# Kernel optimization log

Hardware: AMD Instinct MI355X
Metric: run time of the kernel (lower is better)

## Reference

```python
import jax, jax.numpy as jnp
import numpy as np

NUM_HEADS = 8
NUM_POINTS = 4
NUM_PIP = 4  # num_points_in_pillar
RADIUS = 0.12


def grid_sample_bilinear(feat, grid):
    """torch.nn.functional.grid_sample(mode='bilinear', padding_mode='zeros', align_corners=False).
    feat: [G, D, H, W], grid: [G, Q, P, 2] in [-1, 1] (x=width, y=height) -> [G, Q, P, D]."""
    G, D, H, W = feat.shape
    Q, P = grid.shape[1], grid.shape[2]
    x = (grid[..., 0] + 1.0) * 0.5 * W - 0.5
    y = (grid[..., 1] + 1.0) * 0.5 * H - 0.5
    x0 = jnp.floor(x)
    y0 = jnp.floor(y)
    feat_flat = feat.reshape(G, D, H * W).transpose(0, 2, 1)  # [G, HW, D]
    out = jnp.zeros((G, Q * P, D), dtype=feat.dtype)
    for dx, dy in ((0, 0), (1, 0), (0, 1), (1, 1)):
        xi = x0 + dx
        yi = y0 + dy
        w = (1.0 - jnp.abs(x - xi)) * (1.0 - jnp.abs(y - yi))
        valid = (xi >= 0) & (xi <= W - 1) & (yi >= 0) & (yi <= H - 1)
        xi_c = jnp.clip(xi, 0, W - 1).astype(jnp.int32)
        yi_c = jnp.clip(yi, 0, H - 1).astype(jnp.int32)
        idx = (yi_c * W + xi_c).reshape(G, Q * P)
        g = jnp.take_along_axis(feat_flat, idx[:, :, None], axis=1)  # [G, Q*P, D]
        out = out + g * (w * valid.astype(w.dtype)).reshape(G, Q * P, 1)
    return out.reshape(G, Q, P, D)


def setup_inputs() -> dict:
    key = jax.random.key(0)
    ks = jax.random.split(key, 8)
    B, N, C = 1, 2500, 256
    cams, H, W = 6, 46, 80
    return {
        "query": jax.random.normal(ks[0], (B, N, C), dtype=jnp.float32),
        "image_feats": jax.random.normal(ks[1], (B, cams, C, H, W), dtype=jnp.float32),
        "reference_points_cam": jax.random.uniform(ks[2], (B, cams, N, NUM_PIP, 2), dtype=jnp.float32),
        "bev_mask": jax.random.uniform(ks[3], (B, cams, N, NUM_PIP)) > 0.3,
        "offset_w": jax.random.normal(ks[4], (NUM_HEADS * NUM_PIP * NUM_POINTS * 2, C), dtype=jnp.float32) * 0.02,
        "offset_b": jnp.zeros((NUM_HEADS * NUM_PIP * NUM_POINTS * 2,), dtype=jnp.float32),
        "weight_w": jax.random.normal(ks[5], (NUM_HEADS * NUM_PIP * NUM_POINTS, C), dtype=jnp.float32) * 0.02,
        "weight_b": jnp.zeros((NUM_HEADS * NUM_PIP * NUM_POINTS,), dtype=jnp.float32),
        "out_w": jax.random.normal(ks[6], (C, C), dtype=jnp.float32) * 0.02,
        "out_b": jnp.zeros((C,), dtype=jnp.float32),
    }


def reference(query, image_feats, reference_points_cam, bev_mask,
              offset_w, offset_b, weight_w, weight_b, out_w, out_b):
    B, N, C = query.shape
    cams, H, W = image_feats.shape[1], image_feats.shape[3], image_feats.shape[4]
    heads, PiP, P = NUM_HEADS, NUM_PIP, NUM_POINTS
    K = PiP * P
    D = C // heads

    # Per-query learned offsets and attention logits
    offsets = jnp.tanh(query @ offset_w.T + offset_b).reshape(B, N, heads, PiP, P, 2) * RADIUS
    wl = (query @ weight_w.T + weight_b).reshape(B, N, heads, K)  # [B,N,h,K]

    # Sampling locations per camera: ref [B,cams,N,PiP,2] + offsets -> [B,cams,N,h,K,2]
    loc = reference_points_cam[:, :, :, None, :, None, :] + offsets[:, None]
    loc = loc.reshape(B, cams, N, heads, K, 2)

    # Visibility mask broadcast to points: [B,cams,N,h,K]
    vis = jnp.broadcast_to(bev_mask[:, :, :, None, :, None], (B, cams, N, heads, PiP, P))
    vis = vis.reshape(B, cams, N, heads, K)

    # Masked softmax over K (handles fully-masked rows)
    m = vis.astype(wl.dtype)
    logits = jnp.where(vis, wl[:, None], jnp.asarray(-1e9, wl.dtype))
    w = jax.nn.softmax(logits, axis=-1) * m
    w = w / jnp.clip(jnp.sum(w, axis=-1, keepdims=True), 1e-6)

    # grid_sample over all (batch, cam, head) at once
    grid = loc.transpose(0, 1, 3, 2, 4, 5).reshape(B * cams * heads, N, K, 2) * 2.0 - 1.0
    feat = image_feats.reshape(B * cams * heads, D, H, W)
    sampled = grid_sample_bilinear(feat, grid)  # [B*cams*h, N, K, D]
    sampled = sampled.reshape(B, cams, heads, N, K, D).transpose(0, 1, 3, 2, 4, 5)  # [B,cams,N,h,K,D]

    cam_out = jnp.sum(sampled * w[..., None], axis=4).reshape(B, cams, N, C)

    has_vis = jnp.any(bev_mask, axis=-1)  # [B,cams,N]
    cam_out = cam_out * has_vis[..., None].astype(cam_out.dtype)

    fused = jnp.sum(cam_out, axis=1)  # [B,N,C]
    counts = jnp.clip(jnp.sum(has_vis.astype(jnp.int32), axis=1), 1)  # [B,N]
    fused = fused / counts[..., None].astype(fused.dtype)
    return fused @ out_w.T + out_b
```

## Files before the change

kernel.cpp:

```cpp
#include <hip/hip_runtime.h>
#include <math.h>

#define CAMS 6
#define CCH 256
#define HH 46
#define WW 80
#define NPIX (HH * WW)
#define HEADS 8
#define PIP 4
#define PP 4
#define KK 16
#define RADIUS_F 0.12f
#define NC 384

__device__ __forceinline__ unsigned short f2bf(float f) {
    unsigned int x = __float_as_uint(f);
    unsigned int r = (x + 0x7FFFu + ((x >> 16) & 1u)) >> 16;
    return (unsigned short)r;
}
__device__ __forceinline__ float bf2f(unsigned short u) {
    return __uint_as_float(((unsigned int)u) << 16);
}

__global__ void __launch_bounds__(256) feat_transpose_k(const float* __restrict__ in,
                                                        unsigned short* __restrict__ out) {
    __shared__ float tile[64][65];
    int cam = blockIdx.z;
    int r0 = blockIdx.y * 64;
    int p0 = blockIdx.x * 64;
    int tj = threadIdx.x & 63;
    int ti = threadIdx.x >> 6;
    const float* src = in + ((long)cam * CCH + r0) * NPIX + p0;
#pragma unroll
    for (int k = 0; k < 64; k += 4) {
        if (p0 + tj < NPIX) tile[ti + k][tj] = src[(long)(ti + k) * NPIX + tj];
    }
    __syncthreads();
    unsigned short* dst = out + ((long)cam * NPIX + p0) * CCH + r0;
#pragma unroll
    for (int k = 0; k < 64; k += 4) {
        if (p0 + ti + k < NPIX) dst[(long)(ti + k) * CCH + tj] = f2bf(tile[tj][ti + k]);
    }
}

__global__ void __launch_bounds__(256) wtrans_k(const float* __restrict__ offw,
                                                const float* __restrict__ ww,
                                                const float* __restrict__ outw,
                                                float* __restrict__ WC,
                                                float* __restrict__ outT) {
    __shared__ float tile[64][65];
    int b = blockIdx.x;
    const float* src;
    float* dst;
    int C, tr, tc, dstride, dcol0;
    if (b < 16)      { src = offw; dst = WC;   C = 256; tr = b >> 2;        tc = b & 3;        dstride = NC;  dcol0 = 0; }
    else if (b < 24) { src = ww;   dst = WC;   C = 256; tr = (b - 16) >> 2; tc = (b - 16) & 3; dstride = NC;  dcol0 = 256; }
    else             { src = outw; dst = outT; C = 256; tr = (b - 24) >> 2; tc = (b - 24) & 3; dstride = 256; dcol0 = 0; }
    if (b >= 16 && b < 24) { tr = (b - 16) & 1; tc = (b - 16) >> 1; }
    int tj = threadIdx.x & 63;
    int ti = threadIdx.x >> 6;
#pragma unroll
    for (int k = 0; k < 64; k += 4)
        tile[ti + k][tj] = src[(long)(tr * 64 + ti + k) * C + tc * 64 + tj];
    __syncthreads();
#pragma unroll
    for (int k = 0; k < 64; k += 4)
        dst[(long)(tc * 64 + ti + k) * dstride + dcol0 + tr * 64 + tj] = tile[tj][ti + k];
}

__global__ void __launch_bounds__(256) qgemm3_k(const float* __restrict__ query,
                                                const float* __restrict__ WC,
                                                const float* __restrict__ offB,
                                                const float* __restrict__ wB,
                                                float* __restrict__ offsets,
                                                float* __restrict__ wl,
                                                int N) {
    __shared__ float qt[64][32][4];
    int t = threadIdx.x;
    int w = t >> 6, l = t & 63;
    int m0 = blockIdx.x * 32;
    int col = blockIdx.y * 64 + l;

#pragma unroll
    for (int i = 0; i < 8; i++) {
        int mm = i * 4 + w;
        int gm = m0 + mm;
        float4 v = make_float4(0.f, 0.f, 0.f, 0.f);
        if (gm < N) v = *(const float4*)(query + (long)gm * CCH + (l << 2));
        *(float4*)&qt[l][mm ^ (l & 31)][0] = v;
    }
    __syncthreads();

    int mb = w * 8;
    float acc[8] = {0.f, 0.f, 0.f, 0.f, 0.f, 0.f, 0.f, 0.f};
#pragma unroll 2
    for (int jg = 0; jg < 64; jg++) {
        const float* rp = WC + (long)(jg * 4) * NC + col;
        float w0 = rp[0];
        float w1 = rp[NC];
        float w2 = rp[2 * NC];
        float w3 = rp[3 * NC];
        int sw = jg & 31;
#pragma unroll
        for (int r = 0; r < 8; r++) {
            const float4 qv = *(const float4*)&qt[jg][(mb + r) ^ sw][0];
            acc[r] = fmaf(qv.w, w3, fmaf(qv.z, w2, fmaf(qv.y, w1, fmaf(qv.x, w0, acc[r]))));
        }
    }

    if (col < 256) {
        float b = offB[col];
#pragma unroll
        for (int r = 0; r < 8; r++) {
            int gm = m0 + mb + r;
            if (gm < N) offsets[(long)gm * CCH + col] = tanhf(acc[r] + b) * RADIUS_F;
        }
    } else {
        int c2 = col - 256;
        float b = wB[c2];
#pragma unroll
        for (int r = 0; r < 8; r++) {
            int gm = m0 + mb + r;
            if (gm < N) wl[(long)gm * 128 + c2] = acc[r] + b;
        }
    }
}

__global__ void __launch_bounds__(256, 4) sample_cam_k(
        const unsigned short* __restrict__ feat_t,
        const float* __restrict__ refp,
        const int* __restrict__ bev,
        const float* __restrict__ offsets,
        const float* __restrict__ wl,
        float* __restrict__ cam_out,
        int N, int per_xcd) {
    int xcd = blockIdx.x & 7;
    int local = (blockIdx.x >> 3) * 4 + (threadIdx.x >> 6);
    if (local >= per_xcd) return;
    long task = (long)xcd * per_xcd + local;
    if (task >= (long)CAMS * N) return;
    int cam = (int)(task / N);
    int n = (int)(task - (long)cam * N);

    int l = threadIdx.x & 63;
    int h = l >> 3;

    const int* bv = bev + ((long)cam * N + n) * 4;
    int m0 = bv[0], m1 = bv[1], m2 = bv[2], m3 = bv[3];
    float* outp = cam_out + ((long)cam * N + n) * CCH + (l << 2);
    if (!(m0 | m1 | m2 | m3)) {
        *(float4*)outp = make_float4(0.f, 0.f, 0.f, 0.f);
        return;
    }

    const float* rp = refp + ((long)cam * N + n) * 8;
    const float4* offn = (const float4*)(offsets + (long)n * CCH + (h << 5));
    const float4* wln = (const float4*)(wl + (long)n * 128 + (h << 4));

    float4 wl0, wl1, wl2, wl3;
    float mmax = -1e30f;
    if (m0) { wl0 = wln[0]; mmax = fmaxf(mmax, fmaxf(fmaxf(wl0.x, wl0.y), fmaxf(wl0.z, wl0.w))); }
    if (m1) { wl1 = wln[1]; mmax = fmaxf(mmax, fmaxf(fmaxf(wl1.x, wl1.y), fmaxf(wl1.z, wl1.w))); }
    if (m2) { wl2 = wln[2]; mmax = fmaxf(mmax, fmaxf(fmaxf(wl2.x, wl2.y), fmaxf(wl2.z, wl2.w))); }
    if (m3) { wl3 = wln[3]; mmax = fmaxf(mmax, fmaxf(fmaxf(wl3.x, wl3.y), fmaxf(wl3.z, wl3.w))); }

    float w_[KK];
#pragma unroll
    for (int k = 0; k < KK; k++) w_[k] = 0.f;
    float ssum = 0.f;
    if (m0) {
        w_[0] = __expf(wl0.x - mmax); w_[1] = __expf(wl0.y - mmax);
        w_[2] = __expf(wl0.z - mmax); w_[3] = __expf(wl0.w - mmax);
        ssum += w_[0] + w_[1] + w_[2] + w_[3];
    }
    if (m1) {
        w_[4] = __expf(wl1.x - mmax); w_[5] = __expf(wl1.y - mmax);
        w_[6] = __expf(wl1.z - mmax); w_[7] = __expf(wl1.w - mmax);
        ssum += w_[4] + w_[5] + w_[6] + w_[7];
    }
    if (m2) {
        w_[8] = __expf(wl2.x - mmax); w_[9] = __expf(wl2.y - mmax);
        w_[10] = __expf(wl2.z - mmax); w_[11] = __expf(wl2.w - mmax);
        ssum += w_[8] + w_[9] + w_[10] + w_[11];
    }
    if (m3) {
        w_[12] = __expf(wl3.x - mmax); w_[13] = __expf(wl3.y - mmax);
        w_[14] = __expf(wl3.z - mmax); w_[15] = __expf(wl3.w - mmax);
        ssum += w_[12] + w_[13] + w_[14] + w_[15];
    }
    float inv = 1.f / ssum;

    const ushort4* fcam = (const ushort4*)(feat_t + (long)cam * NPIX * CCH) + l;
    float ax = 0.f, ay = 0.f, az = 0.f, aw = 0.f;

#pragma unroll
    for (int pip = 0; pip < PIP; pip++) {
        int vis = (pip == 0) ? m0 : (pip == 1) ? m1 : (pip == 2) ? m2 : m3;
        if (!vis) continue;
        float rx = rp[pip * 2 + 0];
        float ry = rp[pip * 2 + 1];
        float4 oa = offn[pip * 2];
        float4 ob = offn[pip * 2 + 1];
        float px[PP] = {oa.x, oa.z, ob.x, ob.z};
        float py[PP] = {oa.y, oa.w, ob.y, ob.w};
#pragma unroll
        for (int p = 0; p < PP; p++) {
            float wgt = w_[pip * PP + p];
            float x = fmaf(rx + px[p], (float)WW, -0.5f);
            float y = fmaf(ry + py[p], (float)HH, -0.5f);
            float x0f = floorf(x), y0f = floorf(y);
            float fx = x - x0f, fy = y - y0f;
            int ix = (int)x0f, iy = (int)y0f;
            int ix0 = min(max(ix, 0), WW - 1);
            int ix1 = min(max(ix + 1, 0), WW - 1);
            int iy0 = min(max(iy, 0), HH - 1);
            int iy1 = min(max(iy + 1, 0), HH - 1);
            float wx0 = (1.f - fx) * (((ix >= 0) & (ix < WW)) ? 1.f : 0.f);
            float wx1 = fx * (((ix + 1 >= 0) & (ix + 1 < WW)) ? 1.f : 0.f);
            float wy0 = (1.f - fy) * (((iy >= 0) & (iy < HH)) ? 1.f : 0.f);
            float wy1 = fy * (((iy + 1 >= 0) & (iy + 1 < HH)) ? 1.f : 0.f);
            const ushort4 u00 = fcam[(iy0 * WW + ix0) * (CCH / 4)];
            const ushort4 u01 = fcam[(iy0 * WW + ix1) * (CCH / 4)];
            const ushort4 u10 = fcam[(iy1 * WW + ix0) * (CCH / 4)];
            const ushort4 u11 = fcam[(iy1 * WW + ix1) * (CCH / 4)];
            float a00 = wgt * wy0 * wx0;
            float a01 = wgt * wy0 * wx1;
            float a10 = wgt * wy1 * wx0;
            float a11 = wgt * wy1 * wx1;
            ax = fmaf(a00, bf2f(u00.x), ax); ay = fmaf(a00, bf2f(u00.y), ay);
            az = fmaf(a00, bf2f(u00.z), az); aw = fmaf(a00, bf2f(u00.w), aw);
            ax = fmaf(a01, bf2f(u01.x), ax); ay = fmaf(a01, bf2f(u01.y), ay);
            az = fmaf(a01, bf2f(u01.z), az); aw = fmaf(a01, bf2f(u01.w), aw);
            ax = fmaf(a10, bf2f(u10.x), ax); ay = fmaf(a10, bf2f(u10.y), ay);
            az = fmaf(a10, bf2f(u10.z), az); aw = fmaf(a10, bf2f(u10.w), aw);
            ax = fmaf(a11, bf2f(u11.x), ax); ay = fmaf(a11, bf2f(u11.y), ay);
            az = fmaf(a11, bf2f(u11.z), az); aw = fmaf(a11, bf2f(u11.w), aw);
        }
    }
    *(float4*)outp = make_float4(ax * inv, ay * inv, az * inv, aw * inv);
}

__global__ void __launch_bounds__(256) outproj3_k(const float* __restrict__ cam_out,
                                                  const int* __restrict__ bev,
                                                  const float* __restrict__ outT,
                                                  const float* __restrict__ outB,
                                                  float* __restrict__ out, int N) {
    __shared__ float ft[64][32][4];
    __shared__ float inv_s[32];
    int t = threadIdx.x;
    int w = t >> 6, l = t & 63;
    int m0 = blockIdx.x * 32;
    int col = blockIdx.y * 64 + l;

    if (t < 32) {
        int gm = m0 + t;
        int cnt = 0;
        if (gm < N) {
#pragma unroll
            for (int cam = 0; cam < CAMS; cam++) {
                const int* bv = bev + ((long)cam * N + gm) * 4;
                cnt += (bv[0] | bv[1] | bv[2] | bv[3]) ? 1 : 0;
            }
        }
        inv_s[t] = 1.f / (float)max(cnt, 1);
    }

#pragma unroll
    for (int i = 0; i < 8; i++) {
        int mm = i * 4 + w;
        int gm = m0 + mm;
        float4 s = make_float4(0.f, 0.f, 0.f, 0.f);
        if (gm < N) {
#pragma unroll
            for (int cam = 0; cam < CAMS; cam++) {
                const float4 v = *(const float4*)(cam_out + ((long)cam * N + gm) * CCH + (l << 2));
                s.x += v.x; s.y += v.y; s.z += v.z; s.w += v.w;
            }
        }
        *(float4*)&ft[l][mm ^ (l & 31)][0] = s;
    }
    __syncthreads();

    int mb = w * 8;
    float acc[8] = {0.f, 0.f, 0.f, 0.f, 0.f, 0.f, 0.f, 0.f};
#pragma unroll 2
    for (int jg = 0; jg < 64; jg++) {
        const float* rp = outT + (long)(jg * 4) * CCH + col;
        float w0 = rp[0];
        float w1 = rp[CCH];
        float w2 = rp[2 * CCH];
        float w3 = rp[3 * CCH];
        int sw = jg & 31;
#pragma unroll
        for (int r = 0; r < 8; r++) {
            const float4 qv = *(const float4*)&ft[jg][(mb + r) ^ sw][0];
            acc[r] = fmaf(qv.w, w3, fmaf(qv.z, w2, fmaf(qv.y, w1, fmaf(qv.x, w0, acc[r]))));
        }
    }

    float b = outB[col];
#pragma unroll
    for (int r = 0; r < 8; r++) {
        int gm = m0 + mb + r;
        if (gm < N) out[(long)gm * CCH + col] = fmaf(acc[r], inv_s[mb + r], b);
    }
}

extern "C" void kernel_launch(void* const* d_in, const int* in_sizes, int n_in,
                              void* d_out, int out_size, void* d_ws, size_t ws_size,
                              hipStream_t stream) {
    const float* query    = (const float*)d_in[0];
    const float* imfeat   = (const float*)d_in[1];
    const float* refp     = (const float*)d_in[2];
    const int*   bev      = (const int*)d_in[3];
    const float* offset_w = (const float*)d_in[4];
    const float* offset_b = (const float*)d_in[5];
    const float* weight_w = (const float*)d_in[6];
    const float* weight_b = (const float*)d_in[7];
    const float* out_w    = (const float*)d_in[8];
    const float* out_b    = (const float*)d_in[9];
    float* out = (float*)d_out;

    int N = in_sizes[0] / CCH;

    float* ws = (float*)d_ws;
    unsigned short* feat_t = (unsigned short*)ws;
    float* WC     = ws + (size_t)CAMS * NPIX * CCH / 2;
    float* outT   = WC + (size_t)CCH * NC;
    float* offs   = outT + (size_t)CCH * CCH;
    float* wl     = offs + (size_t)N * CCH;
    float* camob  = wl + (size_t)N * 128;

    feat_transpose_k<<<dim3((NPIX + 63) / 64, CCH / 64, CAMS), 256, 0, stream>>>(imfeat, feat_t);
    wtrans_k<<<40, 256, 0, stream>>>(offset_w, weight_w, out_w, WC, outT);

    int mblocks = (N + 31) / 32;
    qgemm3_k<<<dim3(mblocks, 6), 256, 0, stream>>>(query, WC, offset_b, weight_b, offs, wl, N);

    int T = CAMS * N;
    int per_xcd = (T + 7) / 8;
    int blocks = 8 * ((per_xcd + 3) / 4);
    sample_cam_k<<<blocks, 256, 0, stream>>>(feat_t, refp, bev, offs, wl, camob,
                                             N, per_xcd);

    outproj3_k<<<dim3(mblocks, 4), 256, 0, stream>>>(camob, bev, outT, out_b, out, N);
}
```

Before: 97.14 us.

## Merge prep transposes, drop LDS staging in GEMMs, split camera sum

Merges the feature transpose and weight transpose kernels into a single prep launch. The weights are now stored in an interleaved float4 layout so each GEMM lane loads one float4 per k-group. The query and out-projection GEMMs drop their shared-memory staging and read rows straight from global memory with wave-uniform addresses, which should become scalar or broadcast loads. The six-camera sum moves into its own elementwise kernel that writes an intermediate buffer, so there is one extra launch and an extra global round trip in exchange for a simpler out-projection.

```diff
diff --git a/kernel.cpp b/kernel.cpp
--- a/kernel.cpp
+++ b/kernel.cpp
@@ -12,6 +12,7 @@
 #define KK 16
 #define RADIUS_F 0.12f
 #define NC 384
+#define FEATB (58 * 4 * CAMS)
 
 __device__ __forceinline__ unsigned short f2bf(float f) {
     unsigned int x = __float_as_uint(f);
@@ -22,89 +23,79 @@
     return __uint_as_float(((unsigned int)u) << 16);
 }
 
-__global__ void __launch_bounds__(256) feat_transpose_k(const float* __restrict__ in,
-                                                        unsigned short* __restrict__ out) {
+__global__ void __launch_bounds__(256) prep_k(const float* __restrict__ imfeat,
+                                              unsigned short* __restrict__ feat_t,
+                                              const float* __restrict__ offw,
+                                              const float* __restrict__ ww,
+                                              const float* __restrict__ outw,
+                                              float* __restrict__ WCi,
+                                              float* __restrict__ outTi) {
     __shared__ float tile[64][65];
-    int cam = blockIdx.z;
-    int r0 = blockIdx.y * 64;
-    int p0 = blockIdx.x * 64;
+    int b = blockIdx.x;
     int tj = threadIdx.x & 63;
     int ti = threadIdx.x >> 6;
-    const float* src = in + ((long)cam * CCH + r0) * NPIX + p0;
-#pragma unroll
-    for (int k = 0; k < 64; k += 4) {
-        if (p0 + tj < NPIX) tile[ti + k][tj] = src[(long)(ti + k) * NPIX + tj];
-    }
-    __syncthreads();
-    unsigned short* dst = out + ((long)cam * NPIX + p0) * CCH + r0;
-#pragma unroll
-    for (int k = 0; k < 64; k += 4) {
-        if (p0 + ti + k < NPIX) dst[(long)(ti + k) * CCH + tj] = f2bf(tile[tj][ti + k]);
-    }
-}
-
-__global__ void __launch_bounds__(256) wtrans_k(const float* __restrict__ offw,
-                                                const float* __restrict__ ww,
-                                                const float* __restrict__ outw,
-                                                float* __restrict__ WC,
-                                                float* __restrict__ outT) {
-    __shared__ float tile[64][65];
-    int b = blockIdx.x;
-    const float* src;
-    float* dst;
-    int C, tr, tc, dstride, dcol0;
-    if (b < 16)      { src = offw; dst = WC;   C = 256; tr = b >> 2;        tc = b & 3;        dstride = NC;  dcol0 = 0; }
-    else if (b < 24) { src = ww;   dst = WC;   C = 256; tr = (b - 16) >> 2; tc = (b - 16) & 3; dstride = NC;  dcol0 = 256; }
-    else             { src = outw; dst = outT; C = 256; tr = (b - 24) >> 2; tc = (b - 24) & 3; dstride = 256; dcol0 = 0; }
-    if (b >= 16 && b < 24) { tr = (b - 16) & 1; tc = (b - 16) >> 1; }
-    int tj = threadIdx.x & 63;
-    int ti = threadIdx.x >> 6;
-#pragma unroll
-    for (int k = 0; k < 64; k += 4)
-        tile[ti + k][tj] = src[(long)(tr * 64 + ti + k) * C + tc * 64 + tj];
-    __syncthreads();
-#pragma unroll
-    for (int k = 0; k < 64; k += 4)
-        dst[(long)(tc * 64 + ti + k) * dstride + dcol0 + tr * 64 + tj] = tile[tj][ti + k];
-}
-
-__global__ void __launch_bounds__(256) qgemm3_k(const float* __restrict__ query,
-                                                const float* __restrict__ WC,
+    if (b < FEATB) {
+        int px = b % 58, rest = b / 58;
+        int r0 = (rest % 4) * 64;
+        int cam = rest / 4;
+        int p0 = px * 64;
+        const float* src = imfeat + ((long)cam * CCH + r0) * NPIX + p0;
+#pragma unroll
+        for (int k = 0; k < 64; k += 4) {
+            if (p0 + tj < NPIX) tile[ti + k][tj] = src[(long)(ti + k) * NPIX + tj];
+        }
+        __syncthreads();
+        unsigned short* dst = feat_t + ((long)cam * NPIX + p0) * CCH + r0;
+#pragma unroll
+        for (int k = 0; k < 64; k += 4) {
+            if (p0 + ti + k < NPIX) dst[(long)(ti + k) * CCH + tj] = f2bf(tile[tj][ti + k]);
+        }
+    } else {
+        int c = b - FEATB;
+        const float* src;
+        float* dst;
+        int tr, tc, dcols, dcol0;
+        if (c < 16)      { src = offw; dst = WCi;   tr = c >> 2;        tc = c & 3;         dcols = NC;  dcol0 = 0; }
+        else if (c < 24) { src = ww;   dst = WCi;   tr = (c - 16) & 1;  tc = (c - 16) >> 1; dcols = NC;  dcol0 = 256; }
+        else             { src = outw; dst = outTi; tr = (c - 24) >> 2; tc = (c - 24) & 3;  dcols = 256; dcol0 = 0; }
+#pragma unroll
+        for (int k = 0; k < 64; k += 4)
+            tile[ti + k][tj] = src[(long)(tr * 64 + ti + k) * CCH + tc * 64 + tj];
+        __syncthreads();
+        int col = dcol0 + tr * 64 + tj;
+#pragma unroll
+        for (int q = ti; q < 16; q += 4) {
+            float4 v = make_float4(tile[tj][4 * q + 0], tile[tj][4 * q + 1],
+                                   tile[tj][4 * q + 2], tile[tj][4 * q + 3]);
+            ((float4*)dst)[(long)(tc * 16 + q) * dcols + col] = v;
+        }
+    }
+}
+
+__global__ void __launch_bounds__(256) qgemm4_k(const float* __restrict__ query,
+                                                const float* __restrict__ WCi,
                                                 const float* __restrict__ offB,
                                                 const float* __restrict__ wB,
                                                 float* __restrict__ offsets,
                                                 float* __restrict__ wl,
                                                 int N) {
-    __shared__ float qt[64][32][4];
-    int t = threadIdx.x;
-    int w = t >> 6, l = t & 63;
-    int m0 = blockIdx.x * 32;
+    int w = threadIdx.x >> 6, l = threadIdx.x & 63;
+    int row0 = __builtin_amdgcn_readfirstlane(blockIdx.x * 32 + w * 8);
     int col = blockIdx.y * 64 + l;
 
-#pragma unroll
-    for (int i = 0; i < 8; i++) {
-        int mm = i * 4 + w;
-        int gm = m0 + mm;
-        float4 v = make_float4(0.f, 0.f, 0.f, 0.f);
-        if (gm < N) v = *(const float4*)(query + (long)gm * CCH + (l << 2));
-        *(float4*)&qt[l][mm ^ (l & 31)][0] = v;
-    }
-    __syncthreads();
-
-    int mb = w * 8;
+    const float* qr[8];
+#pragma unroll
+    for (int r = 0; r < 8; r++) qr[r] = query + (long)min(row0 + r, N - 1) * CCH;
+
+    const float4* wp = (const float4*)WCi + col;
     float acc[8] = {0.f, 0.f, 0.f, 0.f, 0.f, 0.f, 0.f, 0.f};
 #pragma unroll 2
     for (int jg = 0; jg < 64; jg++) {
-        const float* rp = WC + (long)(jg * 4) * NC + col;
-        float w0 = rp[0];
-        float w1 = rp[NC];
-        float w2 = rp[2 * NC];
-        float w3 = rp[3 * NC];
-        int sw = jg & 31;
+        float4 wv = wp[(long)jg * NC];
 #pragma unroll
         for (int r = 0; r < 8; r++) {
-            const float4 qv = *(const float4*)&qt[jg][(mb + r) ^ sw][0];
-            acc[r] = fmaf(qv.w, w3, fmaf(qv.z, w2, fmaf(qv.y, w1, fmaf(qv.x, w0, acc[r]))));
+            float4 qv = *(const float4*)(qr[r] + jg * 4);
+            acc[r] = fmaf(qv.w, wv.w, fmaf(qv.z, wv.z, fmaf(qv.y, wv.y, fmaf(qv.x, wv.x, acc[r]))));
         }
     }
 
@@ -112,7 +103,7 @@
         float b = offB[col];
 #pragma unroll
         for (int r = 0; r < 8; r++) {
-            int gm = m0 + mb + r;
+            int gm = row0 + r;
             if (gm < N) offsets[(long)gm * CCH + col] = tanhf(acc[r] + b) * RADIUS_F;
         }
     } else {
@@ -120,7 +111,7 @@
         float b = wB[c2];
 #pragma unroll
         for (int r = 0; r < 8; r++) {
-            int gm = m0 + mb + r;
+            int gm = row0 + r;
             if (gm < N) wl[(long)gm * 128 + c2] = acc[r] + b;
         }
     }
@@ -240,69 +231,62 @@
     *(float4*)outp = make_float4(ax * inv, ay * inv, az * inv, aw * inv);
 }
 
-__global__ void __launch_bounds__(256) outproj3_k(const float* __restrict__ cam_out,
+__global__ void __launch_bounds__(256) camsum_k(const float* __restrict__ cam_out,
+                                                float* __restrict__ fsum, int N) {
+    int idx = blockIdx.x * 256 + threadIdx.x;
+    int total = N * (CCH / 4);
+    if (idx >= total) return;
+    const float4* src = (const float4*)cam_out;
+    float4 s = make_float4(0.f, 0.f, 0.f, 0.f);
+#pragma unroll
+    for (int cam = 0; cam < CAMS; cam++) {
+        float4 v = src[(long)cam * total + idx];
+        s.x += v.x; s.y += v.y; s.z += v.z; s.w += v.w;
+    }
+    ((float4*)fsum)[idx] = s;
+}
+
+__global__ void __launch_bounds__(256) outproj4_k(const float* __restrict__ fsum,
                                                   const int* __restrict__ bev,
-                                                  const float* __restrict__ outT,
+                                                  const float* __restrict__ outTi,
                                                   const float* __restrict__ outB,
                                                   float* __restrict__ out, int N) {
-    __shared__ float ft[64][32][4];
-    __shared__ float inv_s[32];
-    int t = threadIdx.x;
-    int w = t >> 6, l = t & 63;
-    int m0 = blockIdx.x * 32;
+    int w = threadIdx.x >> 6, l = threadIdx.x & 63;
+    int row0 = __builtin_amdgcn_readfirstlane(blockIdx.x * 32 + w * 8);
     int col = blockIdx.y * 64 + l;
 
-    if (t < 32) {
-        int gm = m0 + t;
+    const float* fr[8];
+    float invc[8];
+#pragma unroll
+    for (int r = 0; r < 8; r++) {
+        int rr = min(row0 + r, N - 1);
+        fr[r] = fsum + (long)rr * CCH;
         int cnt = 0;
-        if (gm < N) {
-#pragma unroll
-            for (int cam = 0; cam < CAMS; cam++) {
-                const int* bv = bev + ((long)cam * N + gm) * 4;
-                cnt += (bv[0] | bv[1] | bv[2] | bv[3]) ? 1 : 0;
-            }
-        }
-        inv_s[t] = 1.f / (float)max(cnt, 1);
-    }
-
-#pragma unroll
-    for (int i = 0; i < 8; i++) {
-        int mm = i * 4 + w;
-        int gm = m0 + mm;
-        float4 s = make_float4(0.f, 0.f, 0.f, 0.f);
-        if (gm < N) {
-#pragma unroll
-            for (int cam = 0; cam < CAMS; cam++) {
-                const float4 v = *(const float4*)(cam_out + ((long)cam * N + gm) * CCH + (l << 2));
-                s.x += v.x; s.y += v.y; s.z += v.z; s.w += v.w;
-            }
-        }
-        *(float4*)&ft[l][mm ^ (l & 31)][0] = s;
-    }
-    __syncthreads();
-
-    int mb = w * 8;
+#pragma unroll
+        for (int cam = 0; cam < CAMS; cam++) {
+            const int* bv = bev + ((long)cam * N + rr) * 4;
+            cnt += (bv[0] | bv[1] | bv[2] | bv[3]) ? 1 : 0;
+        }
+        invc[r] = 1.f / (float)max(cnt, 1);
+    }
+
+    const float4* wp = (const float4*)outTi + col;
     float acc[8] = {0.f, 0.f, 0.f, 0.f, 0.f, 0.f, 0.f, 0.f};
 #pragma unroll 2
     for (int jg = 0; jg < 64; jg++) {
-        const float* rp = outT + (long)(jg * 4) * CCH + col;
-        float w0 = rp[0];
-        float w1 = rp[CCH];
-        float w2 = rp[2 * CCH];
-        float w3 = rp[3 * CCH];
-        int sw = jg & 31;
+        float4 wv = wp[(long)jg * CCH];
 #pragma unroll
         for (int r = 0; r < 8; r++) {
-            const float4 qv = *(const float4*)&ft[jg][(mb + r) ^ sw][0];
-            acc[r] = fmaf(qv.w, w3, fmaf(qv.z, w2, fmaf(qv.y, w1, fmaf(qv.x, w0, acc[r]))));
+            float4 qv = *(const float4*)(fr[r] + jg * 4);
+            acc[r] = fmaf(qv.w, wv.w, fmaf(qv.z, wv.z, fmaf(qv.y, wv.y, fmaf(qv.x, wv.x, acc[r]))));
         }
     }
 
     float b = outB[col];
 #pragma unroll
     for (int r = 0; r < 8; r++) {
-        int gm = m0 + mb + r;
-        if (gm < N) out[(long)gm * CCH + col] = fmaf(acc[r], inv_s[mb + r], b);
+        int gm = row0 + r;
+        if (gm < N) out[(long)gm * CCH + col] = fmaf(acc[r], invc[r], b);
     }
 }
 
@@ -325,17 +309,19 @@
 
     float* ws = (float*)d_ws;
     unsigned short* feat_t = (unsigned short*)ws;
-    float* WC     = ws + (size_t)CAMS * NPIX * CCH / 2;
-    float* outT   = WC + (size_t)CCH * NC;
-    float* offs   = outT + (size_t)CCH * CCH;
+    float* WCi    = ws + (size_t)CAMS * NPIX * CCH / 2;
+    float* outTi  = WCi + (size_t)CCH * NC;
+    float* offs   = outTi + (size_t)CCH * CCH;
     float* wl     = offs + (size_t)N * CCH;
     float* camob  = wl + (size_t)N * 128;
-
-    feat_transpose_k<<<dim3((NPIX + 63) / 64, CCH / 64, CAMS), 256, 0, stream>>>(imfeat, feat_t);
-    wtrans_k<<<40, 256, 0, stream>>>(offset_w, weight_w, out_w, WC, outT);
+    float* fsum   = camob + (size_t)CAMS * N * CCH;
+
+    prep_k<<<FEATB + 40, 256, 0, stream>>>(imfeat, feat_t, offset_w, weight_w, out_w,
+                                           WCi, outTi);
 
     int mblocks = (N + 31) / 32;
-    qgemm3_k<<<dim3(mblocks, 6), 256, 0, stream>>>(query, WC, offset_b, weight_b, offs, wl, N);
+    qgemm4_k<<<dim3(mblocks, 6), 256, 0, stream>>>(query, WCi, offset_b, weight_b,
+                                                   offs, wl, N);
 
     int T = CAMS * N;
     int per_xcd = (T + 7) / 8;
@@ -343,5 +329,7 @@
     sample_cam_k<<<blocks, 256, 0, stream>>>(feat_t, refp, bev, offs, wl, camob,
                                              N, per_xcd);
 
-    outproj3_k<<<dim3(mblocks, 4), 256, 0, stream>>>(camob, bev, outT, out_b, out, N);
-}
+    camsum_k<<<(N * (CCH / 4) + 255) / 256, 256, 0, stream>>>(camob, fsum, N);
+
+    outproj4_k<<<dim3(mblocks, 4), 256, 0, stream>>>(fsum, bev, outTi, out_b, out, N);
+}
```

New measurement: 121.2 us. 24.8% more time.
